# Optimization experiments

Hardware: AMD Instinct MI355X
Metric: run time of the kernel (lower is better)

Reference implementation:

```python
import jax, jax.numpy as jnp
import numpy as np

B, INPUTDIM, OUTDIM, GRIDSIZE = 4096, 128, 512, 300

def setup_inputs() -> dict:
    key = jax.random.key(0)
    k1, k2 = jax.random.split(key)
    x = jax.random.normal(k1, (B, INPUTDIM), dtype=jnp.float32)
    scale = 1.0 / (np.sqrt(INPUTDIM) * np.sqrt(GRIDSIZE))
    fouriercoeffs = jax.random.normal(k2, (2, OUTDIM, INPUTDIM, GRIDSIZE), dtype=jnp.float32) * scale
    return {"x": x, "fouriercoeffs": fouriercoeffs}

def reference(x, fouriercoeffs):
    # k: frequencies 1..gridsize
    gridsize = fouriercoeffs.shape[-1]
    k = jnp.arange(1, gridsize + 1, dtype=x.dtype)  # (G,)
    arg = x[:, :, None] * k  # (B, I, G)
    c = jnp.cos(arg)
    s = jnp.sin(arg)
    # einsum('dbik,djik->bj') with d=2 split into cos/sin terms
    y = jnp.einsum('big,jig->bj', c, fouriercoeffs[0]) + jnp.einsum('big,jig->bj', s, fouriercoeffs[1])
    return y
```

## Files before the change

### kernel.cpp

```cpp
#include <hip/hip_runtime.h>
#include <hip/hip_bf16.h>
#include <cstdint>

#define TB 256
#define TBG 512

typedef short short8 __attribute__((ext_vector_type(8)));
typedef float f32x4 __attribute__((ext_vector_type(4)));

constexpr int B_N = 4096, I_N = 128, J_N = 512, G_N = 300;
constexpr int K1 = I_N * G_N;
constexpr int BM = 128, BN = 512;
constexpr int NSP = 8;
constexpr int IC = 16;
constexpr float INV2PI = 0.15915494309189535f;

constexpr int GSTRIDE = 4 * 512 * 8;
constexpr size_t SPSTRIDE = (size_t)G_N * GSTRIDE;

__device__ __forceinline__ ushort f2bf(float f) {
    unsigned int u = __float_as_uint(f);
    return (ushort)((u + 0x7FFFu + ((u >> 16) & 1u)) >> 16);
}

__device__ __forceinline__ float fract_(float x) {
#if __has_builtin(__builtin_amdgcn_fractf)
    return __builtin_amdgcn_fractf(x);
#else
    return x - floorf(x);
#endif
}

__device__ __forceinline__ unsigned int pack_bf2(float a, float b) {
    __hip_bfloat162 h = __float22bfloat162_rn(make_float2(a, b));
    unsigned int u;
    __builtin_memcpy(&u, &h, 4);
    return u;
}

typedef __attribute__((address_space(3))) unsigned int lds_u32_t;
typedef __attribute__((address_space(1))) const unsigned int glb_u32_t;

__device__ __forceinline__ void llds16(const void* g, void* l) {
    __builtin_amdgcn_global_load_lds(
        reinterpret_cast<glb_u32_t*>(reinterpret_cast<uintptr_t>(g)),
        reinterpret_cast<lds_u32_t*>((unsigned int)reinterpret_cast<uintptr_t>(l)),
        16, 0, 0);
}

constexpr int TRG = 60;
constexpr int TRTB = 512;
constexpr int TRUNITS = 256 * 15;

__global__ __launch_bounds__(TRTB) void fkan_tr(const float* __restrict__ src,
                                                ushort* __restrict__ dst,
                                                float* __restrict__ outz) {
    __shared__ __align__(16) ushort L[TRG * 2 * 32 * 8];
    const int gc = blockIdx.x;
    const int sp = blockIdx.y;
    const int djc = blockIdx.z;
    const int dj0 = djc * 32;
    const int d = dj0 >> 9;
    const int j0 = dj0 & 511;
    const int g0 = gc * TRG;
    const int tid = threadIdx.x;

    {
        size_t bid = (size_t)(djc * 8 + sp) * 5 + gc;
        size_t zt = bid * TRTB + tid;
        if (zt < (size_t)B_N * J_N / 4)
            ((float4*)outz)[zt] = make_float4(0.f, 0.f, 0.f, 0.f);
    }

    unsigned int* Lw = (unsigned int*)L;

    auto rbody = [&](int u) {
        int rp = u / 15, c = u - rp * 15;
        int djl = rp >> 3, ilp = rp & 7;
        int ihl = ilp >> 2, e2 = ilp & 3;
        const float* p = src + ((size_t)(dj0 + djl) * 128 + sp * 16 + ilp * 2) * 300
                       + g0 + c * 4;
        float4 va = *(const float4*)p;
        float4 vb = *(const float4*)(p + 300);
        float a[4] = {va.x, va.y, va.z, va.w};
        float b[4] = {vb.x, vb.y, vb.z, vb.w};
        const int swz = (c & 7) << 2;
#pragma unroll
        for (int k = 0; k < 4; ++k) {
            int gl = c * 4 + k;
            int wd = ((gl * 2 + ihl) * 32 + djl) * 4 + e2;
            Lw[wd ^ swz] = pack_bf2(a[k], b[k]);
        }
    };
#pragma unroll
    for (int it = 0; it < 7; ++it) rbody(tid + it * TRTB);
    if (tid < TRUNITS - 7 * TRTB) rbody(tid + 7 * TRTB);
    __syncthreads();

    const uint4* Lv = (const uint4*)L;
    auto wbody = [&](int w) {
        int gl = w >> 6, r = w & 63;
        int ihl = r >> 5, jl = r & 31;
        int q = (gl * 64 + ihl * 32 + jl) ^ ((gl >> 2) & 7);
        size_t d16 = ((size_t)(sp * G_N + g0 + gl) * 4 + d * 2 + ihl) * 512 + j0 + jl;
        ((uint4*)dst)[d16] = Lv[q];
    };
#pragma unroll
    for (int it = 0; it < 7; ++it) wbody(tid + it * TRTB);
    if (tid < TRG * 64 - 7 * TRTB) wbody(tid + 7 * TRTB);
}

__global__ __launch_bounds__(TBG, 2)
void fkan_gemm(const float* __restrict__ x,
               const ushort* __restrict__ fcb,
               float* __restrict__ out) {
    __shared__ __align__(16) ushort At[2 * 4 * 128 * 8];
    __shared__ __align__(16) ushort Bt[2 * 4 * 512 * 8];

    const int tid = threadIdx.x;
    const int bm = blockIdx.x, sp = blockIdx.z;
    const int lane = tid & 63, wid = tid >> 6;
    const int wm = wid & 1, wn = wid >> 1;
    const int lhi = lane >> 4, llo = lane & 15;
    const int m = tid & 127, q4 = tid >> 7;
    const int ihq = q4 >> 1, eq = (q4 & 1) * 4;

    float sv[4], cv[4], s0[4], c0[4];
    {
        const float* xr = x + ((size_t)(bm * BM + m)) * I_N + sp * IC + q4 * 4;
        float4 xa = *(const float4*)xr;
        float xv[4] = {xa.x, xa.y, xa.z, xa.w};
#pragma unroll
        for (int j = 0; j < 4; ++j) {
            float r = fract_(xv[j] * INV2PI);
            s0[j] = __builtin_amdgcn_sinf(r);
            c0[j] = __builtin_amdgcn_cosf(r);
            sv[j] = s0[j];
            cv[j] = c0[j];
        }
    }

    const ushort* bp[4];
#pragma unroll
    for (int p = 0; p < 4; ++p)
        bp[p] = fcb + (size_t)sp * SPSTRIDE
              + ((size_t)((wid >> 1) * 512 + (wid & 1) * 256 + p * 64 + lane)) * 8;

    const int aoff = (lhi * 128 + wm * 64 + llo) * 8;
    const int boff = (lhi * 512 + wn * 128 + llo) * 8;
    ushort* awc0 = &At[(ihq * 128 + m) * 8 + eq];
    ushort* aws0 = &At[((2 + ihq) * 128 + m) * 8 + eq];

    f32x4 acc[4][8];
#pragma unroll
    for (int a = 0; a < 4; ++a)
#pragma unroll
        for (int b = 0; b < 8; ++b) acc[a][b] = (f32x4){0.f, 0.f, 0.f, 0.f};

    auto stageB = [&](int nb) {
#pragma unroll
        for (int p = 0; p < 4; ++p) {
            llds16(bp[p], (char*)Bt
                       + (size_t)(nb * 2048 + (wid >> 1) * 512 + (wid & 1) * 256 + p * 64) * 16);
            bp[p] += GSTRIDE;
        }
    };
    auto writeA = [&](int nb) {
        uint2 vc = {pack_bf2(cv[0], cv[1]), pack_bf2(cv[2], cv[3])};
        *(uint2*)(awc0 + nb * 4096) = vc;
        uint2 vs = {pack_bf2(sv[0], sv[1]), pack_bf2(sv[2], sv[3])};
        *(uint2*)(aws0 + nb * 4096) = vs;
#pragma unroll
        for (int j = 0; j < 4; ++j) {
            float t = __builtin_fmaf(sv[j], c0[j], cv[j] * s0[j]);
            cv[j] = __builtin_fmaf(cv[j], c0[j], -(sv[j] * s0[j]));
            sv[j] = t;
        }
    };
    auto halfstep = [&](int cb, bool doNext) {
        __syncthreads();
        short8 af[4], bfr[8];
#pragma unroll
        for (int t = 0; t < 4; ++t)
            af[t] = *(const short8*)&At[cb * 4096 + aoff + t * 128];
#pragma unroll
        for (int t = 0; t < 8; ++t)
            bfr[t] = *(const short8*)&Bt[cb * 16384 + boff + t * 128];
        if (doNext) stageB(cb ^ 1);
#pragma unroll
        for (int tm = 0; tm < 4; ++tm)
#pragma unroll
            for (int tn = 0; tn < 8; ++tn)
                acc[tm][tn] = __builtin_amdgcn_mfma_f32_16x16x32_bf16(
                    af[tm], bfr[tn], acc[tm][tn], 0, 0, 0);
        if (doNext) writeA(cb ^ 1);
    };

    writeA(0);
    stageB(0);

    for (int g = 0; g < G_N; g += 2) {
        halfstep(0, true);
        halfstep(1, g + 2 < G_N);
    }

    const int row0 = bm * BM + wm * 64 + lhi * 4;
    const int col0 = wn * 128 + llo;
#pragma unroll
    for (int tm = 0; tm < 4; ++tm)
#pragma unroll
        for (int tn = 0; tn < 8; ++tn)
#pragma unroll
            for (int r = 0; r < 4; ++r)
                atomicAdd(&out[(size_t)(row0 + tm * 16 + r) * J_N + col0 + tn * 16],
                          acc[tm][tn][r]);
}

constexpr int SPL_FB = 4;
constexpr int KS_FB = 2 * K1 / SPL_FB;
constexpr int NSTEP_FB = KS_FB / 32;

__global__ __launch_bounds__(TB)
void fkan_gemm_fb(const float* __restrict__ x,
                  const float* __restrict__ fc32,
                  float* __restrict__ out) {
    __shared__ float xs[128][65];
    __shared__ __align__(16) ushort At[4 * 128 * 8];
    __shared__ __align__(16) ushort Bt[4 * 128 * 8];

    const int tid = threadIdx.x;
    const int bm = blockIdx.x, bn = blockIdx.y, sp = blockIdx.z;
    const int d = sp >> 1;
    const int ib = (sp & 1) << 6;
    const int rbase = ib * G_N;

    for (int idx = tid; idx < 128 * 64; idx += TB) {
        int row = idx >> 6, il = idx & 63;
        xs[row][il] = x[(size_t)(bm * 128 + row) * I_N + ib + il];
    }

    f32x4 acc[4][4];
#pragma unroll
    for (int a = 0; a < 4; ++a)
#pragma unroll
        for (int b = 0; b < 4; ++b) acc[a][b] = (f32x4){0.f, 0.f, 0.f, 0.f};

    const int lane = tid & 63, wid = tid >> 6;
    const int wm = wid & 1, wn = wid >> 1;
    const int lhi = lane >> 4, llo = lane & 15;
    const int am = tid & 127, akg0 = tid >> 7;

    const float* f32base = fc32 + ((size_t)d * J_N + bn * 128) * K1 + rbase;

    for (int step = 0; step < NSTEP_FB; ++step) {
        __syncthreads();
#pragma unroll
        for (int it = 0; it < 2; ++it) {
            const int kg = akg0 + it * 2;
            int r = rbase + step * 32 + kg * 8;
            int i = (int)((unsigned)r / 300u);
            int g = r - i * 300;
            float xxv = xs[am][i - ib];
            float kkf = (float)(g + 1);
            short8 avv;
#pragma unroll
            for (int j = 0; j < 8; ++j) {
                float rev = xxv * kkf * INV2PI;
                float fr = fract_(rev) + (d ? 0.0f : 0.25f);
                avv[j] = (short)f2bf(__builtin_amdgcn_sinf(fract_(fr)));
                if (j < 7) {
                    ++g; kkf += 1.0f;
                    if (g == 300) { g = 0; kkf = 1.0f; ++i; xxv = xs[am][i - ib]; }
                }
            }
            *(short8*)&At[(kg * 128 + am) * 8] = avv;
        }
#pragma unroll
        for (int it = 0; it < 2; ++it) {
            int item = tid + it * TB;
            int n = item >> 2, grp = item & 3;
            const float* gp = f32base + (size_t)n * K1 + step * 32 + grp * 8;
            float4 v0 = *(const float4*)gp;
            float4 v1 = *(const float4*)(gp + 4);
            short8 bv;
            bv[0] = (short)f2bf(v0.x); bv[1] = (short)f2bf(v0.y);
            bv[2] = (short)f2bf(v0.z); bv[3] = (short)f2bf(v0.w);
            bv[4] = (short)f2bf(v1.x); bv[5] = (short)f2bf(v1.y);
            bv[6] = (short)f2bf(v1.z); bv[7] = (short)f2bf(v1.w);
            *(short8*)&Bt[(grp * 128 + n) * 8] = bv;
        }
        __syncthreads();
        short8 af[4], bf[4];
#pragma unroll
        for (int t = 0; t < 4; ++t) {
            af[t] = *(const short8*)&At[(lhi * 128 + wm * 64 + t * 16 + llo) * 8];
            bf[t] = *(const short8*)&Bt[(lhi * 128 + wn * 64 + t * 16 + llo) * 8];
        }
#pragma unroll
        for (int tm = 0; tm < 4; ++tm)
#pragma unroll
            for (int tn = 0; tn < 4; ++tn)
                acc[tm][tn] = __builtin_amdgcn_mfma_f32_16x16x32_bf16(
                    af[tm], bf[tn], acc[tm][tn], 0, 0, 0);
    }

    const int row0 = bm * 128 + wm * 64 + lhi * 4;
    const int col0 = bn * 128 + wn * 64 + llo;
#pragma unroll
    for (int tm = 0; tm < 4; ++tm)
#pragma unroll
        for (int tn = 0; tn < 4; ++tn)
#pragma unroll
            for (int r = 0; r < 4; ++r)
                atomicAdd(&out[(size_t)(row0 + tm * 16 + r) * J_N + col0 + tn * 16],
                          acc[tm][tn][r]);
}

extern "C" void kernel_launch(void* const* d_in, const int* in_sizes, int n_in,
                              void* d_out, int out_size, void* d_ws, size_t ws_size,
                              hipStream_t stream) {
    const float* x = (const float*)d_in[0];
    const float* fc = (const float*)d_in[1];
    float* out = (float*)d_out;

    const size_t need = (size_t)2 * J_N * K1 * sizeof(ushort);

    if (ws_size >= need) {
        ushort* fcb = (ushort*)d_ws;
        fkan_tr<<<dim3(5, 8, 32), TRTB, 0, stream>>>(fc, fcb, out);
        dim3 grid(B_N / BM, 1, NSP);
        fkan_gemm<<<grid, TBG, 0, stream>>>(x, fcb, out);
    } else {
        hipMemsetAsync(d_out, 0, (size_t)out_size * sizeof(float), stream);
        dim3 grid(B_N / 128, J_N / 128, SPL_FB);
        fkan_gemm_fb<<<grid, TB, 0, stream>>>(x, fc, out);
    }
}
```

Before: 528.8 us.

## Load B fragments directly into registers, drop LDS staging for coefficients

The B operand (Fourier coefficients) is no longer staged through LDS. Each wave now loads its own 64-column slice of B straight from global memory into registers, double-buffered across steps. The warp tiling changes from 2x4 (64x128 per wave) to 1x8 (128 rows x 64 columns per wave), so B data is not shared between waves. This removes the LDS write/read traffic and LDS footprint for B. In exchange it relies on global load latency being hidden by register prefetch, and it reads 16-byte B fragments per lane less coalesced. The A write mapping is also changed to m=tid>>2.

```diff
diff --git a/kernel.cpp b/kernel.cpp
--- a/kernel.cpp
+++ b/kernel.cpp
@@ -115,14 +115,14 @@
                const ushort* __restrict__ fcb,
                float* __restrict__ out) {
     __shared__ __align__(16) ushort At[2 * 4 * 128 * 8];
-    __shared__ __align__(16) ushort Bt[2 * 4 * 512 * 8];
 
     const int tid = threadIdx.x;
     const int bm = blockIdx.x, sp = blockIdx.z;
     const int lane = tid & 63, wid = tid >> 6;
-    const int wm = wid & 1, wn = wid >> 1;
     const int lhi = lane >> 4, llo = lane & 15;
-    const int m = tid & 127, q4 = tid >> 7;
+
+    const int m = tid >> 2;
+    const int q4 = tid & 3;
     const int ihq = q4 >> 1, eq = (q4 & 1) * 4;
 
     float sv[4], cv[4], s0[4], c0[4];
@@ -140,31 +140,26 @@
         }
     }
 
-    const ushort* bp[4];
-#pragma unroll
-    for (int p = 0; p < 4; ++p)
-        bp[p] = fcb + (size_t)sp * SPSTRIDE
-              + ((size_t)((wid >> 1) * 512 + (wid & 1) * 256 + p * 64 + lane)) * 8;
-
-    const int aoff = (lhi * 128 + wm * 64 + llo) * 8;
-    const int boff = (lhi * 512 + wn * 128 + llo) * 8;
     ushort* awc0 = &At[(ihq * 128 + m) * 8 + eq];
     ushort* aws0 = &At[((2 + ihq) * 128 + m) * 8 + eq];
 
-    f32x4 acc[4][8];
-#pragma unroll
-    for (int a = 0; a < 4; ++a)
-#pragma unroll
-        for (int b = 0; b < 8; ++b) acc[a][b] = (f32x4){0.f, 0.f, 0.f, 0.f};
-
-    auto stageB = [&](int nb) {
-#pragma unroll
-        for (int p = 0; p < 4; ++p) {
-            llds16(bp[p], (char*)Bt
-                       + (size_t)(nb * 2048 + (wid >> 1) * 512 + (wid & 1) * 256 + p * 64) * 16);
-            bp[p] += GSTRIDE;
-        }
-    };
+    const ushort* bbase = fcb + (size_t)sp * SPSTRIDE
+                        + ((size_t)lhi * 512 + wid * 64 + llo) * 8;
+    auto loadB = [&](short8* br, int g) {
+        const ushort* p = bbase + (size_t)g * GSTRIDE;
+#pragma unroll
+        for (int t = 0; t < 4; ++t)
+            br[t] = *(const short8*)(p + t * 128);
+    };
+
+    const int aoff = (lhi * 128 + llo) * 8;
+
+    f32x4 acc[8][4];
+#pragma unroll
+    for (int a = 0; a < 8; ++a)
+#pragma unroll
+        for (int b = 0; b < 4; ++b) acc[a][b] = (f32x4){0.f, 0.f, 0.f, 0.f};
+
     auto writeA = [&](int nb) {
         uint2 vc = {pack_bf2(cv[0], cv[1]), pack_bf2(cv[2], cv[3])};
         *(uint2*)(awc0 + nb * 4096) = vc;
@@ -177,39 +172,39 @@
             sv[j] = t;
         }
     };
-    auto halfstep = [&](int cb, bool doNext) {
+
+    short8 bA[4], bB[4];
+
+    auto halfstep = [&](int cb, short8* bcur, short8* bnxt, int gnext, bool doNext) {
         __syncthreads();
-        short8 af[4], bfr[8];
-#pragma unroll
-        for (int t = 0; t < 4; ++t)
+        if (doNext) loadB(bnxt, gnext);
+        short8 af[8];
+#pragma unroll
+        for (int t = 0; t < 8; ++t)
             af[t] = *(const short8*)&At[cb * 4096 + aoff + t * 128];
 #pragma unroll
-        for (int t = 0; t < 8; ++t)
-            bfr[t] = *(const short8*)&Bt[cb * 16384 + boff + t * 128];
-        if (doNext) stageB(cb ^ 1);
-#pragma unroll
-        for (int tm = 0; tm < 4; ++tm)
-#pragma unroll
-            for (int tn = 0; tn < 8; ++tn)
+        for (int tm = 0; tm < 8; ++tm)
+#pragma unroll
+            for (int tn = 0; tn < 4; ++tn)
                 acc[tm][tn] = __builtin_amdgcn_mfma_f32_16x16x32_bf16(
-                    af[tm], bfr[tn], acc[tm][tn], 0, 0, 0);
+                    af[tm], bcur[tn], acc[tm][tn], 0, 0, 0);
         if (doNext) writeA(cb ^ 1);
     };
 
     writeA(0);
-    stageB(0);
+    loadB(bA, 0);
 
     for (int g = 0; g < G_N; g += 2) {
-        halfstep(0, true);
-        halfstep(1, g + 2 < G_N);
-    }
-
-    const int row0 = bm * BM + wm * 64 + lhi * 4;
-    const int col0 = wn * 128 + llo;
-#pragma unroll
-    for (int tm = 0; tm < 4; ++tm)
-#pragma unroll
-        for (int tn = 0; tn < 8; ++tn)
+        halfstep(0, bA, bB, g + 1, true);
+        halfstep(1, bB, bA, g + 2, g + 2 < G_N);
+    }
+
+    const int row0 = bm * BM + lhi * 4;
+    const int col0 = wid * 64 + llo;
+#pragma unroll
+    for (int tm = 0; tm < 8; ++tm)
+#pragma unroll
+        for (int tn = 0; tn < 4; ++tn)
 #pragma unroll
             for (int r = 0; r < 4; ++r)
                 atomicAdd(&out[(size_t)(row0 + tm * 16 + r) * J_N + col0 + tn * 16],
```

Result: no change. 529.6 us (+0.2%).
